# Kernel tuning notes

Measured on AMD Instinct MI355X. Metric: run time of the kernel, lower is better.

The kernel has to match this reference:

```python
import jax, jax.numpy as jnp
import numpy as np

N_CLASS, N_SUPPORT, N_QUERY = 5, 5, 15
C, T, V = 128, 8, 25
LN_EPS = 1e-12


def setup_inputs() -> dict:
    key = jax.random.key(0)
    ks = jax.random.split(key, 6)
    n_tot = N_CLASS * (N_SUPPORT + N_QUERY)
    inp = jax.random.normal(ks[0], (n_tot, C, T, V), dtype=jnp.float32)
    # episode labels: 20 consecutive samples per class (arange // per_class)
    target = (jnp.arange(n_tot, dtype=jnp.int32) // (N_SUPPORT + N_QUERY)).astype(jnp.int32)
    s = 0.02
    p = lambda k: jax.random.normal(k, (C, C), dtype=jnp.float32) * s
    return {
        'input': inp,
        'Wq': p(ks[1]), 'bq': jnp.zeros((C,), jnp.float32),
        'Wk': p(ks[2]), 'bk': jnp.zeros((C,), jnp.float32),
        'Wv': p(ks[3]), 'bv': jnp.zeros((C,), jnp.float32),
        'Wo': p(ks[4]), 'bo': jnp.zeros((C,), jnp.float32),
        'ln_g': jnp.ones((C,), jnp.float32), 'ln_b': jnp.zeros((C,), jnp.float32),
        'target': target,
        'n_support': N_SUPPORT,
    }


def _layer_norm(x, g, b):
    mu = x.mean(-1, keepdims=True)
    var = ((x - mu) ** 2).mean(-1, keepdims=True)
    return (x - mu) * jax.lax.rsqrt(var + LN_EPS) * g + b


def _episode_forward(input, Wq, bq, Wk, bk, Wv, bv, Wo, bo, ln_g, ln_b, target, n_support):
    n_tot, c, t, v = input.shape
    m = N_CLASS
    per_class = n_tot // m
    n_query = per_class - n_support
    n = m * n_query

    # support/query split (stable argsort == torch.where per class for sorted labels)
    order = jnp.argsort(target).reshape(m, per_class)
    supp_idx = order[:, :n_support]                      # (m, h)
    qry_idx = order[:, n_support:].reshape(-1)           # (n,)
    z_proto = input[supp_idx]                            # (m, h, c, t, v)
    zq = input[qry_idx]                                  # (n, c, t, v)

    # ---- hal(): pairwise cross-attention over the vertex axis ----
    mh = m * n_support
    zq_p = jnp.transpose(zq, (0, 2, 3, 1))                                   # (n, t, v, c)
    zp_p = jnp.transpose(z_proto.reshape(mh, c, t, v), (0, 2, 3, 1))          # (mh, t, v, c)
    cat = jnp.concatenate([zq_p, zp_p], axis=0)                               # (n1, t, v, c)
    n1 = cat.shape[0]

    # Q from each of the n1 items, K/V from each of the mh prototypes.
    # Equivalent to the original expand->reshape pairing, without duplicating K/V.
    Q = cat @ Wq + bq                                                         # (n1, t, v, c)
    K = zp_p @ Wk + bk                                                        # (mh, t, v, c)
    Vv = zp_p @ Wv + bv                                                       # (mh, t, v, c)
    scale = 1.0 / jnp.sqrt(jnp.asarray(c, dtype=Q.dtype))
    scores = jnp.einsum('ntqc,mtkc->nmtqk', Q, K) * scale                     # (n1, mh, t, v, v)
    attn = jax.nn.softmax(scores, axis=-1)
    ctx = jnp.einsum('nmtqk,mtkc->nmtqc', attn, Vv)                           # (n1, mh, t, v, c)
    out = _layer_norm(ctx @ Wo + bo + cat[:, None], ln_g, ln_b)               # residual + LN
    att = out.mean(axis=1)                                                    # (n1, t, v, c) mean over mh pairs

    zq_att = jnp.transpose(att[:n], (0, 3, 1, 2))                             # (n, c, t, v)
    proto_att = att[n:].reshape(m, n_support, t, v, c).mean(axis=1)           # (m, t, v, c)
    proto_att = jnp.transpose(proto_att, (0, 3, 1, 2))                        # (m, c, t, v)

    # ---- squared-Euclidean metric on flattened features ----
    zq_f = zq_att.reshape(n, -1)
    zp_f = proto_att.reshape(m, -1)
    dist = jnp.sum((zq_f[:, None, :] - zp_f[None, :, :]) ** 2, axis=-1)       # (n, m)

    log_p_y = jax.nn.log_softmax(-dist, axis=1).reshape(m, n_query, m)
    cls = jnp.arange(m)
    loss = -log_p_y[cls[:, None], jnp.arange(n_query)[None, :], cls[:, None]].mean()
    y_hat = jnp.argmax(log_p_y, axis=2)
    acc = (y_hat == cls[:, None]).astype(jnp.float32).mean()
    return loss, acc


def reference(input, Wq, bq, Wk, bk, Wv, bv, Wo, bo, ln_g, ln_b, target, n_support):
    return _episode_forward(input, Wq, bq, Wk, bk, Wv, bv, Wo, bo, ln_g, ln_b, target, n_support)
```

## Files before the change

### kernel.cpp

```cpp
#include <hip/hip_runtime.h>
#include <math.h>

#define NTOT 100
#define NQ   75
#define NP   25
#define CC   128
#define TT   8
#define VV   25
#define NCLS 5
#define NSUP 5
#define NQRY 15
#define ROW  (TT*VV*CC)
#define TILE (VV*CC)
#define ROWS_Q 20000
#define ROWS_S 5000
#define RB_Q 625
#define RB_S 157

typedef __attribute__((ext_vector_type(8))) short short8;
typedef __attribute__((ext_vector_type(16))) float f32x16;

typedef union { uint4 u4; short8 s8; } pk_t;

__device__ __forceinline__ ushort f2bf(float f) {
    uint u = __float_as_uint(f);
    u += 0x7FFFu + ((u >> 16) & 1u);
    return (ushort)(u >> 16);
}
__device__ __forceinline__ float bf2f(uint u16v) {
    return __uint_as_float(u16v << 16);
}
__device__ __forceinline__ uint pkbf(float a, float b) {
    return (uint)f2bf(a) | ((uint)f2bf(b) << 16);
}

__global__ __launch_bounds__(256) void k_proj(
    const float* __restrict__ input, const int* __restrict__ target,
    const float* __restrict__ Wq, const float* __restrict__ Wk,
    const float* __restrict__ Wv, const float* __restrict__ Wo,
    const float* __restrict__ bq, const float* __restrict__ bk,
    const float* __restrict__ bv,
    ushort* __restrict__ catC, ushort* __restrict__ Qf,
    ushort* __restrict__ Kf, ushort* __restrict__ Vf,
    int* __restrict__ counter) {
    __shared__ ushort stage[32 * 132];
    __shared__ ushort Wf[16384];
    __shared__ ushort VtF[4096];
    __shared__ int iscr[200];

    int bid = blockIdx.x, tid = threadIdx.x;
    int w = tid >> 6, lane = tid & 63, half = lane >> 5, l31 = lane & 31;

    if (bid == 0 && tid == 0) *counter = 0;

    if (tid < NTOT) iscr[tid] = target[tid];
    __syncthreads();
    if (tid < NTOT) {
        int ti = iscr[tid], rank = 0;
        for (int j = 0; j < NTOT; ++j) {
            int tj = iscr[j];
            rank += (tj < ti) || (tj == ti && j < tid);
        }
        iscr[100 + rank] = tid;
    }
    __syncthreads();

    bool isQ = bid < RB_Q;
    int rowblk = isQ ? bid : bid - RB_Q;
    int rlimit = isQ ? ROWS_Q : ROWS_S;
    int g0 = rowblk * 32;
    int gend = min(g0 + 32, rlimit);

    for (int nn = g0 / 200; nn <= (gend - 1) / 200; ++nn) {
        int lo = max(g0 - nn * 200, 0);
        int hi = min(gend - 1 - nn * 200, 199);
        int len = hi - lo + 1;
        int nidx = isQ ? nn : (NQ + nn);
        int src;
        if (nidx < NQ) { int m = nidx / NQRY, qq = nidx - m * NQRY; src = iscr[100 + m * 20 + NSUP + qq]; }
        else           { int i2 = nidx - NQ; int m = i2 / NSUP, s = i2 - m * NSUP; src = iscr[100 + m * 20 + s]; }
        const float* inb = input + (size_t)src * ROW + lo;
        int rbase = nn * 200 + lo - g0;
        for (int idx = tid; idx < len * 128; idx += 256) {
            int c = idx / len, k = idx - c * len;
            stage[(rbase + k) * 132 + c] = f2bf(inb[c * 200 + k]);
        }
    }

    #define BUILDW(W) do {                                                       \
        for (int o = tid; o < 2048; o += 256) {                                  \
            int k8 = o >> 7, c = o & 127;                                        \
            uint4 pk;                                                            \
            pk.x = pkbf((W)[(k8*8+0)*128 + c], (W)[(k8*8+1)*128 + c]);           \
            pk.y = pkbf((W)[(k8*8+2)*128 + c], (W)[(k8*8+3)*128 + c]);           \
            pk.z = pkbf((W)[(k8*8+4)*128 + c], (W)[(k8*8+5)*128 + c]);           \
            pk.w = pkbf((W)[(k8*8+6)*128 + c], (W)[(k8*8+7)*128 + c]);           \
            int dst = (((c >> 5) * 8 + (k8 >> 1)) * 64 + ((c & 31) + 32 * (k8 & 1))) * 8; \
            *(uint4*)(Wf + dst) = pk;                                            \
        }                                                                        \
    } while (0)

    BUILDW(isQ ? Wq : Wk);
    __syncthreads();

    short8 af[8];
    #pragma unroll
    for (int ks = 0; ks < 8; ++ks)
        af[ks] = *(const short8*)&stage[l31 * 132 + ks * 16 + half * 8];

    #define CHAIN(A, OUT) do {                                                   \
        const ushort* bp_ = Wf + w * 4096 + lane * 8;                            \
        _Pragma("unroll")                                                        \
        for (int ks = 0; ks < 8; ++ks) {                                         \
            short8 bf_ = *(const short8*)(bp_ + ks * 512);                       \
            OUT = __builtin_amdgcn_mfma_f32_32x32x16_bf16(A[ks], bf_, OUT, 0, 0, 0); \
        }                                                                        \
    } while (0)

    if (isQ) {
        f32x16 Cm;
        #pragma unroll
        for (int r = 0; r < 16; ++r) Cm[r] = 0.f;
        CHAIN(af, Cm);
        float bcol = bq[w * 32 + l31];
        int c = w * 32 + l31;
        #pragma unroll
        for (int r = 0; r < 16; ++r) {
            int row = g0 + (r & 3) + 8 * (r >> 2) + 4 * half;
            int st = row / 25, vv = row - st * 25;
            size_t dst = (((size_t)st * 8 + (c >> 4)) * 64 + (vv + 32 * ((c >> 3) & 1))) * 8 + (c & 7);
            Qf[dst] = f2bf(Cm[r] + bcol);
        }
        uint* cc = (uint*)catC + (size_t)g0 * 64;
        for (int idx = tid; idx < 2048; idx += 256) {
            int row = idx >> 6, c2 = (idx & 63) * 2;
            cc[idx] = (uint)stage[row * 132 + c2] | ((uint)stage[row * 132 + c2 + 1] << 16);
        }
    } else {
        {
            f32x16 Cm;
            #pragma unroll
            for (int r = 0; r < 16; ++r) Cm[r] = 0.f;
            CHAIN(af, Cm);
            float bcol = bk[w * 32 + l31];
            int c = w * 32 + l31;
            #pragma unroll
            for (int r = 0; r < 16; ++r) {
                int row = g0 + (r & 3) + 8 * (r >> 2) + 4 * half;
                if (row < ROWS_S) {
                    int st = row / 25, vv = row - st * 25;
                    size_t dst = (((size_t)st * 8 + (c >> 4)) * 64 + (vv + 32 * ((c >> 3) & 1))) * 8 + (c & 7);
                    Kf[dst] = f2bf(Cm[r] + bcol);
                }
            }
        }
        __syncthreads();
        BUILDW(Wv);
        __syncthreads();
        {
            f32x16 Cm;
            #pragma unroll
            for (int r = 0; r < 16; ++r) Cm[r] = 0.f;
            CHAIN(af, Cm);
            float bcol = bv[w * 32 + l31];
            int c = w * 32 + l31;
            int ks2 = c >> 4, kh = (c >> 3) & 1, j2 = c & 7;
            #pragma unroll
            for (int r = 0; r < 16; ++r) {
                int rowLocal = (r & 3) + 8 * (r >> 2) + 4 * half;
                VtF[ks2 * 512 + (rowLocal + 32 * kh) * 8 + j2] = f2bf(Cm[r] + bcol);
            }
        }
        __syncthreads();
        BUILDW(Wo);
        __syncthreads();
        short8 a2[8];
        #pragma unroll
        for (int ks = 0; ks < 8; ++ks)
            a2[ks] = *(const short8*)&VtF[ks * 512 + lane * 8];
        {
            f32x16 Cm;
            #pragma unroll
            for (int r = 0; r < 16; ++r) Cm[r] = 0.f;
            CHAIN(a2, Cm);
            int c = w * 32 + l31;
            #pragma unroll
            for (int r = 0; r < 16; ++r) {
                int row = g0 + (r & 3) + 8 * (r >> 2) + 4 * half;
                if (row < ROWS_S) {
                    int tile = row / 25, vv = row - tile * 25;
                    size_t dst = ((((size_t)tile * 4 + (c >> 5)) * 2 + (vv >> 4)) * 64
                                  + ((c & 31) + 32 * ((vv & 15) >> 3))) * 8 + (vv & 7);
                    Vf[dst] = f2bf(Cm[r]);
                }
            }
        }
    }
    #undef CHAIN
    #undef BUILDW
}

__global__ __launch_bounds__(256, 2) void k_attn(
    const ushort* __restrict__ Qf, const ushort* __restrict__ Kf,
    const ushort* __restrict__ Vf, const ushort* __restrict__ catC,
    const float* __restrict__ bo, float* __restrict__ att) {
    __shared__ union {
        struct {
            float catb[25 * 129];
            ushort qls[4096];
        } loop;
        float red[50][66];
    } sm;

    int pair = blockIdx.x;
    int t = pair & 7;
    int tid = threadIdx.x;
    int wv = tid >> 6, lane = tid & 63;
    int q = lane & 31, half = lane >> 5;

    {
        const uint* cc = (const uint*)catC + (size_t)pair * 1600;
        for (int i2 = tid; i2 < 1600; i2 += 256) {
            uint u = cc[i2];
            int r = i2 >> 6, c2 = (i2 & 63) * 2;
            sm.loop.catb[r * 129 + c2]     = bf2f(u & 0xffffu) + bo[c2];
            sm.loop.catb[r * 129 + c2 + 1] = bf2f(u >> 16) + bo[c2 + 1];
        }
    }
    {
        const uint* qp = (const uint*)(Qf + (size_t)pair * 4096);
        uint* ql = (uint*)sm.loop.qls;
        for (int i2 = tid; i2 < 2048; i2 += 256) ql[i2] = qp[i2];
    }
    __syncthreads();

    int qc = q < 25 ? q : 24;
    float attsum[64];
    #pragma unroll
    for (int i = 0; i < 64; ++i) attsum[i] = 0.f;
    float Csc = 0.f;

    const float CEXP = (float)(1.4426950408889634 * 0.08838834764831845);

    const ushort* kbase = Kf + (size_t)t * 4096 + lane * 8;
    short8 kf[8];
    #pragma unroll
    for (int ks = 0; ks < 8; ++ks)
        kf[ks] = *(const short8*)(kbase + (size_t)wv * 32768 + ks * 512);

    int cnt = (wv == 0) ? 7 : 6;
    for (int mi = 0; mi < cnt; ++mi) {
        int m = wv + 4 * mi;

        f32x16 S;
        #pragma unroll
        for (int r = 0; r < 16; ++r) S[r] = 0.f;
        #pragma unroll
        for (int ks = 0; ks < 8; ++ks) {
            short8 qv = *(const short8*)(sm.loop.qls + ks * 512 + lane * 8);
            S = __builtin_amdgcn_mfma_f32_32x32x16_bf16(kf[ks], qv, S, 0, 0, 0);
        }

        float p[16], mx = -3e38f;
        #pragma unroll
        for (int r = 0; r < 16; ++r) {
            int key = (r & 3) + 8 * (r >> 2) + 4 * half;
            float v = (key < 25) ? S[r] : -3e38f;
            p[r] = v; mx = fmaxf(mx, v);
        }
        mx = fmaxf(mx, __shfl_xor(mx, 32));
        float sum = 0.f;
        #pragma unroll
        for (int r = 0; r < 16; ++r) { p[r] = exp2f((p[r] - mx) * CEXP); sum += p[r]; }
        sum += __shfl_xor(sum, 32);
        float inv = 1.f / sum;

        const ushort* vp = Vf + ((size_t)(m * 8 + t)) * 4096 + lane * 8;
        short8 vf0 = *(const short8*)(vp);
        short8 vf1 = *(const short8*)(vp + 512);
        short8 vf2 = *(const short8*)(vp + 1024);
        short8 vf3 = *(const short8*)(vp + 1536);
        short8 vf4 = *(const short8*)(vp + 2048);
        short8 vf5 = *(const short8*)(vp + 2560);
        short8 vf6 = *(const short8*)(vp + 3072);
        short8 vf7 = *(const short8*)(vp + 3584);
        #pragma unroll
        for (int ks = 0; ks < 8; ++ks)
            kf[ks] = *(const short8*)(kbase + (size_t)(m + 4) * 32768 + ks * 512);

        uint o01   = pkbf(p[0] * inv,  p[1] * inv);
        uint o23   = pkbf(p[2] * inv,  p[3] * inv);
        uint o45   = pkbf(p[4] * inv,  p[5] * inv);
        uint o67   = pkbf(p[6] * inv,  p[7] * inv);
        uint o89   = pkbf(p[8] * inv,  p[9] * inv);
        uint o1011 = pkbf(p[10] * inv, p[11] * inv);
        uint o1213 = pkbf(p[12] * inv, p[13] * inv);
        uint o1415 = pkbf(p[14] * inv, p[15] * inv);
        bool h0 = (half == 0);
        uint rA = __shfl_xor(h0 ? o45 : o01, 32);
        uint rB = __shfl_xor(h0 ? o67 : o23, 32);
        uint rC = __shfl_xor(h0 ? o1213 : o89, 32);
        uint rD = __shfl_xor(h0 ? o1415 : o1011, 32);
        pk_t P0, P1;
        P0.u4 = h0 ? make_uint4(o01, o23, rA, rB) : make_uint4(rA, rB, o45, o67);
        P1.u4 = h0 ? make_uint4(o89, o1011, rC, rD) : make_uint4(rC, rD, o1213, o1415);
        short8 pb0 = P0.s8, pb1 = P1.s8;

        f32x16 ctx[4];
        #pragma unroll
        for (int mt = 0; mt < 4; ++mt) {
            #pragma unroll
            for (int r = 0; r < 16; ++r) ctx[mt][r] = 0.f;
        }
        ctx[0] = __builtin_amdgcn_mfma_f32_32x32x16_bf16(vf0, pb0, ctx[0], 0, 0, 0);
        ctx[0] = __builtin_amdgcn_mfma_f32_32x32x16_bf16(vf1, pb1, ctx[0], 0, 0, 0);
        ctx[1] = __builtin_amdgcn_mfma_f32_32x32x16_bf16(vf2, pb0, ctx[1], 0, 0, 0);
        ctx[1] = __builtin_amdgcn_mfma_f32_32x32x16_bf16(vf3, pb1, ctx[1], 0, 0, 0);
        ctx[2] = __builtin_amdgcn_mfma_f32_32x32x16_bf16(vf4, pb0, ctx[2], 0, 0, 0);
        ctx[2] = __builtin_amdgcn_mfma_f32_32x32x16_bf16(vf5, pb1, ctx[2], 0, 0, 0);
        ctx[3] = __builtin_amdgcn_mfma_f32_32x32x16_bf16(vf6, pb0, ctx[3], 0, 0, 0);
        ctx[3] = __builtin_amdgcn_mfma_f32_32x32x16_bf16(vf7, pb1, ctx[3], 0, 0, 0);

        float s1 = 0.f, s2 = 0.f;
        #pragma unroll
        for (int mt = 0; mt < 4; ++mt) {
            float t1 = 0.f, t2 = 0.f;
            #pragma unroll
            for (int r = 0; r < 16; ++r) {
                int c = mt * 32 + (r & 3) + 8 * (r >> 2) + 4 * half;
                float xv = ctx[mt][r] + sm.loop.catb[qc * 129 + c];
                ctx[mt][r] = xv;
                t1 += xv; t2 = fmaf(xv, xv, t2);
            }
            s1 += t1; s2 += t2;
        }
        s1 += __shfl_xor(s1, 32); s2 += __shfl_xor(s2, 32);
        float mu = s1 * (1.f / 128.f);
        float var = s2 * (1.f / 128.f) - mu * mu;
        var = fmaxf(var, 0.f);
        float rs = rsqrtf(var + 1e-12f);
        #pragma unroll
        for (int i = 0; i < 64; ++i)
            attsum[i] = fmaf(ctx[i >> 4][i & 15], rs, attsum[i]);
        Csc = fmaf(-mu, rs, Csc);
    }

    __syncthreads();
    int s = half * 25 + q;
    bool act = q < 25;
    if (wv == 3 && act) {
        #pragma unroll
        for (int i = 0; i < 64; ++i) sm.red[s][i] = attsum[i];
        sm.red[s][64] = Csc;
    }
    __syncthreads();
    if (wv == 2 && act) {
        #pragma unroll
        for (int i = 0; i < 64; ++i) attsum[i] += sm.red[s][i];
        Csc += sm.red[s][64];
    }
    __syncthreads();
    if (wv == 2 && act) {
        #pragma unroll
        for (int i = 0; i < 64; ++i) sm.red[s][i] = attsum[i];
        sm.red[s][64] = Csc;
    }
    __syncthreads();
    if (wv == 0 && act) {
        #pragma unroll
        for (int i = 0; i < 64; ++i) attsum[i] += sm.red[s][i];
        Csc += sm.red[s][64];
    }
    __syncthreads();
    if (wv == 1 && act) {
        #pragma unroll
        for (int i = 0; i < 64; ++i) sm.red[s][i] = attsum[i];
        sm.red[s][64] = Csc;
    }
    __syncthreads();
    if (wv == 0 && act) {
        #pragma unroll
        for (int i = 0; i < 64; ++i) attsum[i] += sm.red[s][i];
        Csc += sm.red[s][64];
        float* ap = att + (size_t)pair * TILE + q * 128;
        #pragma unroll
        for (int mt = 0; mt < 4; ++mt) {
            #pragma unroll
            for (int rg4 = 0; rg4 < 4; ++rg4) {
                int c0 = mt * 32 + 8 * rg4 + 4 * half;
                int i0 = mt * 16 + rg4 * 4;
                float4 o;
                o.x = attsum[i0 + 0] + Csc; o.y = attsum[i0 + 1] + Csc;
                o.z = attsum[i0 + 2] + Csc; o.w = attsum[i0 + 3] + Csc;
                *(float4*)&ap[c0] = o;
            }
        }
    }
}

__global__ __launch_bounds__(256) void k_dist_loss(
    const float* __restrict__ att, const float* __restrict__ ln_g,
    float* __restrict__ dist, int* __restrict__ counter,
    float* __restrict__ out) {
    int b = blockIdx.x;
    int i = b / 5, j = b - 5 * i;
    const float4* a  = (const float4*)(att + (size_t)i * ROW);
    const float4* s0 = (const float4*)(att + (size_t)(NQ + j * 5 + 0) * ROW);
    const float4* s1p = (const float4*)(att + (size_t)(NQ + j * 5 + 1) * ROW);
    const float4* s2p = (const float4*)(att + (size_t)(NQ + j * 5 + 2) * ROW);
    const float4* s3p = (const float4*)(att + (size_t)(NQ + j * 5 + 3) * ROW);
    const float4* s4p = (const float4*)(att + (size_t)(NQ + j * 5 + 4) * ROW);
    float d = 0.f;
    for (int e4 = threadIdx.x; e4 < 6400; e4 += 256) {
        float4 av = a[e4];
        float4 q0 = s0[e4], q1 = s1p[e4], q2 = s2p[e4], q3 = s3p[e4], q4 = s4p[e4];
        float4 g4 = *(const float4*)(ln_g + (e4 & 31) * 4);
        float px = 0.2f * (q0.x + q1.x + q2.x + q3.x + q4.x);
        float py = 0.2f * (q0.y + q1.y + q2.y + q3.y + q4.y);
        float pz = 0.2f * (q0.z + q1.z + q2.z + q3.z + q4.z);
        float pw = 0.2f * (q0.w + q1.w + q2.w + q3.w + q4.w);
        float dx = av.x - px, dy = av.y - py, dz = av.z - pz, dw = av.w - pw;
        d = fmaf(g4.x * g4.x, dx * dx, d);
        d = fmaf(g4.y * g4.y, dy * dy, d);
        d = fmaf(g4.z * g4.z, dz * dz, d);
        d = fmaf(g4.w * g4.w, dw * dw, d);
    }
    #pragma unroll
    for (int msk = 32; msk >= 1; msk >>= 1) d += __shfl_xor(d, msk);
    __shared__ float part[4];
    __shared__ int lastFlag;
    int lane = threadIdx.x & 63, wv = threadIdx.x >> 6;
    if (lane == 0) part[wv] = d;
    __syncthreads();
    if (threadIdx.x == 0) {
        float total = (part[0] + part[1] + part[2] + part[3]) * (1.f / 625.f);
        __hip_atomic_store(&dist[b], total, __ATOMIC_RELEASE, __HIP_MEMORY_SCOPE_AGENT);
        int tk = __hip_atomic_fetch_add(counter, 1, __ATOMIC_ACQ_REL, __HIP_MEMORY_SCOPE_AGENT);
        lastFlag = (tk == 374);
    }
    __syncthreads();
    if (!lastFlag) return;

    int iq = threadIdx.x;
    float li = 0.f, ok = 0.f;
    if (iq < NQ) {
        float dd[5];
        #pragma unroll
        for (int jj = 0; jj < 5; ++jj)
            dd[jj] = __hip_atomic_load(&dist[iq * 5 + jj], __ATOMIC_ACQUIRE, __HIP_MEMORY_SCOPE_AGENT);
        int cls = iq / NQRY;
        float mind = dd[0];
        int best = 0;
        #pragma unroll
        for (int jj = 1; jj < 5; ++jj) {
            if (dd[jj] < mind) mind = dd[jj];
            if (dd[jj] < dd[best]) best = jj;
        }
        float sume = 0.f;
        #pragma unroll
        for (int jj = 0; jj < 5; ++jj) sume += expf(mind - dd[jj]);
        float lse = logf(sume) - mind;
        li = dd[cls] + lse;
        ok = (best == cls) ? 1.f : 0.f;
    }
    #pragma unroll
    for (int msk = 32; msk >= 1; msk >>= 1) {
        li += __shfl_xor(li, msk);
        ok += __shfl_xor(ok, msk);
    }
    if (lane == 0) { part[wv] = li; part[wv + 2] = ok; }
    __syncthreads();
    if (threadIdx.x == 0) {
        out[0] = (part[0] + part[1]) / 75.f;
        out[1] = (part[2] + part[3]) / 75.f;
    }
}

extern "C" void kernel_launch(void* const* d_in, const int* in_sizes, int n_in,
                              void* d_out, int out_size, void* d_ws, size_t ws_size,
                              hipStream_t stream) {
    const float* input = (const float*)d_in[0];
    const float* Wq   = (const float*)d_in[1];
    const float* bq   = (const float*)d_in[2];
    const float* Wk   = (const float*)d_in[3];
    const float* bk   = (const float*)d_in[4];
    const float* Wv   = (const float*)d_in[5];
    const float* bv   = (const float*)d_in[6];
    const float* Wo   = (const float*)d_in[7];
    const float* bo   = (const float*)d_in[8];
    const float* ln_g = (const float*)d_in[9];
    const float* ln_b = (const float*)d_in[10];
    const int* target = (const int*)d_in[11];
    float* out = (float*)d_out;
    (void)ln_b;

    float* ws = (float*)d_ws;
    ushort* catC = (ushort*)ws;
    ushort* Qf   = catC + 2560000;
    ushort* Kf   = Qf + 3276800;
    ushort* Vf   = Kf + 819200;
    float*  att  = (float*)(Vf + 819200);
    float*  distb = att + 2560000;
    int*    counter = (int*)(distb + 512);

    k_proj<<<RB_Q + RB_S, 256, 0, stream>>>(input, target, Wq, Wk, Wv, Wo, bq, bk, bv,
                                            catC, Qf, Kf, Vf, counter);
    k_attn<<<800, 256, 0, stream>>>(Qf, Kf, Vf, catC, bo, att);
    k_dist_loss<<<375, 256, 0, stream>>>(att, ln_g, distb, counter, out);
}
```

Baseline: 185.2 us.

## Accumulate class prototypes with atomics in attention, compute five distances per query block

The attention kernel now folds the support-item outputs straight into per-class prototype buffers using scaled atomicAdd, instead of writing them to the att buffer. The projection kernel zeroes those buffers first. The distance kernel then launches one block per query rather than one per query-class pair, and each block reads the query row once against five precomputed prototypes. This removes the repeated five-way support averaging and the redundant query reads, at the cost of float atomic contention in the attention epilogue and a nondeterministic summation order.

```diff
diff --git a/kernel.cpp b/kernel.cpp
--- a/kernel.cpp
+++ b/kernel.cpp
@@ -42,7 +42,7 @@
     const float* __restrict__ bv,
     ushort* __restrict__ catC, ushort* __restrict__ Qf,
     ushort* __restrict__ Kf, ushort* __restrict__ Vf,
-    int* __restrict__ counter) {
+    float* __restrict__ proto, int* __restrict__ counter) {
     __shared__ ushort stage[32 * 132];
     __shared__ ushort Wf[16384];
     __shared__ ushort VtF[4096];
@@ -70,6 +70,12 @@
     int rlimit = isQ ? ROWS_Q : ROWS_S;
     int g0 = rowblk * 32;
     int gend = min(g0 + 32, rlimit);
+
+    if (!isQ) {
+        int idx0 = rowblk * 816;
+        for (int i2 = idx0 + tid; i2 < idx0 + 816 && i2 < NCLS * ROW; i2 += 256)
+            proto[i2] = 0.f;
+    }
 
     for (int nn = g0 / 200; nn <= (gend - 1) / 200; ++nn) {
         int lo = max(g0 - nn * 200, 0);
@@ -203,17 +209,18 @@
 __global__ __launch_bounds__(256, 2) void k_attn(
     const ushort* __restrict__ Qf, const ushort* __restrict__ Kf,
     const ushort* __restrict__ Vf, const ushort* __restrict__ catC,
-    const float* __restrict__ bo, float* __restrict__ att) {
+    const float* __restrict__ bo, float* __restrict__ att,
+    float* __restrict__ proto) {
     __shared__ union {
         struct {
+            ushort qls[4096];
             float catb[25 * 129];
-            ushort qls[4096];
         } loop;
         float red[50][66];
     } sm;
 
     int pair = blockIdx.x;
-    int t = pair & 7;
+    int n = pair >> 3, t = pair & 7;
     int tid = threadIdx.x;
     int wv = tid >> 6, lane = tid & 63;
     int q = lane & 31, half = lane >> 5;
@@ -382,61 +389,77 @@
         #pragma unroll
         for (int i = 0; i < 64; ++i) attsum[i] += sm.red[s][i];
         Csc += sm.red[s][64];
-        float* ap = att + (size_t)pair * TILE + q * 128;
-        #pragma unroll
-        for (int mt = 0; mt < 4; ++mt) {
-            #pragma unroll
-            for (int rg4 = 0; rg4 < 4; ++rg4) {
-                int c0 = mt * 32 + 8 * rg4 + 4 * half;
-                int i0 = mt * 16 + rg4 * 4;
-                float4 o;
-                o.x = attsum[i0 + 0] + Csc; o.y = attsum[i0 + 1] + Csc;
-                o.z = attsum[i0 + 2] + Csc; o.w = attsum[i0 + 3] + Csc;
-                *(float4*)&ap[c0] = o;
+        if (n < NQ) {
+            float* ap = att + (size_t)pair * TILE + q * 128;
+            #pragma unroll
+            for (int mt = 0; mt < 4; ++mt) {
+                #pragma unroll
+                for (int rg4 = 0; rg4 < 4; ++rg4) {
+                    int c0 = mt * 32 + 8 * rg4 + 4 * half;
+                    int i0 = mt * 16 + rg4 * 4;
+                    float4 o;
+                    o.x = attsum[i0 + 0] + Csc; o.y = attsum[i0 + 1] + Csc;
+                    o.z = attsum[i0 + 2] + Csc; o.w = attsum[i0 + 3] + Csc;
+                    *(float4*)&ap[c0] = o;
+                }
             }
+        } else {
+            int cls = (n - NQ) / NSUP;
+            float* pp = proto + (size_t)cls * ROW + t * TILE + q * 128;
+            #pragma unroll
+            for (int mt = 0; mt < 4; ++mt) {
+                #pragma unroll
+                for (int r = 0; r < 16; ++r) {
+                    int c = mt * 32 + (r & 3) + 8 * (r >> 2) + 4 * half;
+                    atomicAdd(&pp[c], (attsum[mt * 16 + r] + Csc) * 0.2f);
+                }
+            }
         }
     }
 }
 
 __global__ __launch_bounds__(256) void k_dist_loss(
-    const float* __restrict__ att, const float* __restrict__ ln_g,
-    float* __restrict__ dist, int* __restrict__ counter,
-    float* __restrict__ out) {
-    int b = blockIdx.x;
-    int i = b / 5, j = b - 5 * i;
-    const float4* a  = (const float4*)(att + (size_t)i * ROW);
-    const float4* s0 = (const float4*)(att + (size_t)(NQ + j * 5 + 0) * ROW);
-    const float4* s1p = (const float4*)(att + (size_t)(NQ + j * 5 + 1) * ROW);
-    const float4* s2p = (const float4*)(att + (size_t)(NQ + j * 5 + 2) * ROW);
-    const float4* s3p = (const float4*)(att + (size_t)(NQ + j * 5 + 3) * ROW);
-    const float4* s4p = (const float4*)(att + (size_t)(NQ + j * 5 + 4) * ROW);
-    float d = 0.f;
+    const float* __restrict__ att, const float* __restrict__ proto,
+    const float* __restrict__ ln_g, float* __restrict__ dist,
+    int* __restrict__ counter, float* __restrict__ out) {
+    int i = blockIdx.x;
+    const float4* a = (const float4*)(att + (size_t)i * ROW);
+    float d[5] = {0.f, 0.f, 0.f, 0.f, 0.f};
     for (int e4 = threadIdx.x; e4 < 6400; e4 += 256) {
         float4 av = a[e4];
-        float4 q0 = s0[e4], q1 = s1p[e4], q2 = s2p[e4], q3 = s3p[e4], q4 = s4p[e4];
         float4 g4 = *(const float4*)(ln_g + (e4 & 31) * 4);
-        float px = 0.2f * (q0.x + q1.x + q2.x + q3.x + q4.x);
-        float py = 0.2f * (q0.y + q1.y + q2.y + q3.y + q4.y);
-        float pz = 0.2f * (q0.z + q1.z + q2.z + q3.z + q4.z);
-        float pw = 0.2f * (q0.w + q1.w + q2.w + q3.w + q4.w);
-        float dx = av.x - px, dy = av.y - py, dz = av.z - pz, dw = av.w - pw;
-        d = fmaf(g4.x * g4.x, dx * dx, d);
-        d = fmaf(g4.y * g4.y, dy * dy, d);
-        d = fmaf(g4.z * g4.z, dz * dz, d);
-        d = fmaf(g4.w * g4.w, dw * dw, d);
-    }
-    #pragma unroll
-    for (int msk = 32; msk >= 1; msk >>= 1) d += __shfl_xor(d, msk);
-    __shared__ float part[4];
+        float gx = g4.x * g4.x, gy = g4.y * g4.y, gz = g4.z * g4.z, gw = g4.w * g4.w;
+        #pragma unroll
+        for (int j = 0; j < 5; ++j) {
+            float4 pv = *(const float4*)(proto + (size_t)j * ROW + e4 * 4);
+            float dx = av.x - pv.x, dy = av.y - pv.y, dz = av.z - pv.z, dw = av.w - pv.w;
+            d[j] = fmaf(gx, dx * dx, d[j]);
+            d[j] = fmaf(gy, dy * dy, d[j]);
+            d[j] = fmaf(gz, dz * dz, d[j]);
+            d[j] = fmaf(gw, dw * dw, d[j]);
+        }
+    }
+    __shared__ float part[4][5];
     __shared__ int lastFlag;
     int lane = threadIdx.x & 63, wv = threadIdx.x >> 6;
-    if (lane == 0) part[wv] = d;
+    #pragma unroll
+    for (int j = 0; j < 5; ++j) {
+        #pragma unroll
+        for (int msk = 32; msk >= 1; msk >>= 1) d[j] += __shfl_xor(d[j], msk);
+    }
+    if (lane == 0) {
+        #pragma unroll
+        for (int j = 0; j < 5; ++j) part[wv][j] = d[j];
+    }
     __syncthreads();
     if (threadIdx.x == 0) {
-        float total = (part[0] + part[1] + part[2] + part[3]) * (1.f / 625.f);
-        __hip_atomic_store(&dist[b], total, __ATOMIC_RELEASE, __HIP_MEMORY_SCOPE_AGENT);
+        #pragma unroll
+        for (int j = 0; j < 5; ++j) {
+            float total = (part[0][j] + part[1][j] + part[2][j] + part[3][j]) * (1.f / 625.f);
+            __hip_atomic_store(&dist[i * 5 + j], total, __ATOMIC_RELEASE, __HIP_MEMORY_SCOPE_AGENT);
+        }
         int tk = __hip_atomic_fetch_add(counter, 1, __ATOMIC_ACQ_REL, __HIP_MEMORY_SCOPE_AGENT);
-        lastFlag = (tk == 374);
+        lastFlag = (tk == NQ - 1);
     }
     __syncthreads();
     if (!lastFlag) return;
@@ -468,11 +491,11 @@
         li += __shfl_xor(li, msk);
         ok += __shfl_xor(ok, msk);
     }
-    if (lane == 0) { part[wv] = li; part[wv + 2] = ok; }
+    if (lane == 0) { part[wv][0] = li; part[wv][1] = ok; }
     __syncthreads();
     if (threadIdx.x == 0) {
-        out[0] = (part[0] + part[1]) / 75.f;
-        out[1] = (part[2] + part[3]) / 75.f;
+        out[0] = (part[0][0] + part[1][0] + part[2][0] + part[3][0]) / 75.f;
+        out[1] = (part[0][1] + part[1][1] + part[2][1] + part[3][1]) / 75.f;
     }
 }
 
@@ -500,11 +523,12 @@
     ushort* Kf   = Qf + 3276800;
     ushort* Vf   = Kf + 819200;
     float*  att  = (float*)(Vf + 819200);
-    float*  distb = att + 2560000;
+    float*  proto = att + 1920000;
+    float*  distb = proto + 128000;
     int*    counter = (int*)(distb + 512);
 
     k_proj<<<RB_Q + RB_S, 256, 0, stream>>>(input, target, Wq, Wk, Wv, Wo, bq, bk, bv,
-                                            catC, Qf, Kf, Vf, counter);
-    k_attn<<<800, 256, 0, stream>>>(Qf, Kf, Vf, catC, bo, att);
-    k_dist_loss<<<375, 256, 0, stream>>>(att, ln_g, distb, counter, out);
-}
+                                            catC, Qf, Kf, Vf, proto, counter);
+    k_attn<<<800, 256, 0, stream>>>(Qf, Kf, Vf, catC, bo, att, proto);
+    k_dist_loss<<<NQ, 256, 0, stream>>>(att, proto, ln_g, distb, counter, out);
+}
```

Result: slower. 193.5 us (+4.5%).
